# Kernel optimization log

Measured on AMD Instinct MI355X. Metric: run time of the kernel, lower is better.

## Reference

```python
import jax, jax.numpy as jnp
import numpy as np

DIM = 128      # embedding dim (c)
HEAD_DIM = 32
NH = DIM // HEAD_DIM          # 4 mLSTM heads
INNER = 256                    # round_up(2*DIM, 64)
DH = INNER // NH               # 64 per-head dim
K = 4                          # causal conv kernel size
BS = 4                         # qkv_proj_blocksize
NB = INNER // BS               # 64 block-diagonal qkv blocks
B, T, H, W = 8, 16, 32, 32


def setup_inputs() -> dict:
    key = jax.random.key(0)
    ks = jax.random.split(key, 12)
    s = 0.02
    return {
        "x": jax.random.normal(ks[0], (B, DIM, T, H, W), jnp.float32),
        "W_up": jax.random.normal(ks[1], (DIM, 2 * INNER), jnp.float32) * s,
        "conv_w": jax.random.normal(ks[2], (K, 1, INNER), jnp.float32) * s,  # depthwise causal conv (WIO)
        "conv_b": jnp.zeros((INNER,), jnp.float32),
        "Wq": jax.random.normal(ks[3], (NB, BS, BS), jnp.float32) * s,  # block-diag headwise linear
        "Wk": jax.random.normal(ks[4], (NB, BS, BS), jnp.float32) * s,
        "Wv": jax.random.normal(ks[5], (NB, BS, BS), jnp.float32) * s,
        "ig_w": jax.random.normal(ks[6], (3 * INNER, NH), jnp.float32) * s,
        "ig_b": jnp.zeros((NH,), jnp.float32),
        "fg_w": jax.random.normal(ks[7], (3 * INNER, NH), jnp.float32) * s,
        "fg_b": jnp.zeros((NH,), jnp.float32),
        "ln_w": jnp.ones((INNER,), jnp.float32),   # multi-head layernorm scale
        "skip": jnp.ones((INNER,), jnp.float32),   # learnable skip
        "W_down": jax.random.normal(ks[8], (INNER, DIM), jnp.float32) * s,
    }


def _headwise(y, Wh):
    # block-diagonal linear: y [B,S,INNER] split into NB blocks of BS
    Bx, S, _ = y.shape
    yb = y.reshape(Bx, S, NB, BS)
    return jnp.einsum('bsni,noi->bsno', yb, Wh).reshape(Bx, S, INNER)


def _mlstm_parallel(q, k, v, ig, fg):
    # q,k,v: [B,NH,S,DH]; ig,fg (gate preacts): [B,NH,S]
    S = q.shape[2]
    log_f = jax.nn.log_sigmoid(fg)
    lf_cum = jnp.concatenate(
        [jnp.zeros_like(log_f[..., :1]), jnp.cumsum(log_f, axis=-1)], axis=-1)  # [B,NH,S+1]
    logfg = lf_cum[..., 1:, None] - lf_cum[..., None, 1:]                      # [B,NH,S,S]
    mask = jnp.tril(jnp.ones((S, S), bool))
    logfg = jnp.where(mask, logfg, -jnp.inf)
    log_D = logfg + ig[..., None, :]
    max_log_D = jnp.max(log_D, axis=-1, keepdims=True)
    Dmat = jnp.exp(log_D - max_log_D)
    qk = jnp.einsum('bhsd,bhtd->bhst', q, k) / jnp.sqrt(jnp.float32(q.shape[-1]))
    C = qk * Dmat
    normalizer = jnp.maximum(jnp.abs(C.sum(-1, keepdims=True)), jnp.exp(-max_log_D))
    return jnp.einsum('bhst,bhtd->bhsd', C / (normalizer + 1e-6), v)


def _forward(x, W_up, conv_w, conv_b, Wq, Wk, Wv, ig_w, ig_b, fg_w, fg_b, ln_w, skip, W_down):
    b, c, t, hh, ww = x.shape
    xs = jnp.transpose(x, (0, 3, 4, 2, 1)).reshape(b * hh * ww, t, c)  # (b h w) t c
    up = xs @ W_up
    x_m, z = jnp.split(up, 2, axis=-1)                                  # [Bx,S,INNER] each
    # depthwise causal conv + swish
    xc = jax.lax.conv_general_dilated(
        x_m, conv_w, (1,), [(K - 1, 0)],
        dimension_numbers=('NWC', 'WIO', 'NWC'), feature_group_count=INNER) + conv_b
    xc = jax.nn.silu(xc)
    q = _headwise(xc, Wq)
    k = _headwise(xc, Wk)
    v = _headwise(x_m, Wv)
    if_in = jnp.concatenate([q, k, v], axis=-1)
    ig = if_in @ ig_w + ig_b                                            # [Bx,S,NH]
    fg = if_in @ fg_w + fg_b
    Bx, S = q.shape[0], q.shape[1]
    qh = q.reshape(Bx, S, NH, DH).transpose(0, 2, 1, 3)
    kh = k.reshape(Bx, S, NH, DH).transpose(0, 2, 1, 3)
    vh = v.reshape(Bx, S, NH, DH).transpose(0, 2, 1, 3)
    ht = _mlstm_parallel(qh, kh, vh, ig.transpose(0, 2, 1), fg.transpose(0, 2, 1))  # [Bx,NH,S,DH]
    # multi-head (group) layernorm over DH, weight only
    mu = ht.mean(-1, keepdims=True)
    var = ht.var(-1, keepdims=True)
    hn = (ht - mu) / jnp.sqrt(var + 1e-5) * ln_w.reshape(NH, DH)[None, :, None, :]
    hn = hn.transpose(0, 2, 1, 3).reshape(Bx, S, INNER)
    h_state = (hn + skip * xc) * jax.nn.silu(z)
    out = h_state @ W_down                                              # [Bx,S,DIM]
    return out.reshape(b, hh, ww, t, c).transpose(0, 4, 3, 1, 2)        # b c t h w


def reference(x, W_up, conv_w, conv_b, Wq, Wk, Wv, ig_w, ig_b, fg_w, fg_b, ln_w, skip, W_down):
    return _forward(x, W_up, conv_w, conv_b, Wq, Wk, Wv, ig_w, ig_b, fg_w, fg_b, ln_w, skip, W_down)
```

## Files before the change

kernel.cpp:

```cpp
#include <hip/hip_runtime.h>
#include <hip/hip_bf16.h>
#include <cmath>


typedef __attribute__((ext_vector_type(8))) short short8;
typedef __attribute__((ext_vector_type(4))) short short4v;
typedef __attribute__((ext_vector_type(4))) float f32x4;
typedef unsigned short ushort_t;

static __device__ __forceinline__ float siluf(float v) {
  return v / (1.0f + __expf(-v));
}
static __device__ __forceinline__ float logsigf(float v) {
  return fminf(v, 0.f) - log1pf(__expf(-fabsf(v)));
}
static __device__ __forceinline__ float sel4(float4 w, int idx) {
  float r = w.x;
  r = (idx == 1) ? w.y : r;
  r = (idx == 2) ? w.z : r;
  r = (idx == 3) ? w.w : r;
  return r;
}
static __device__ __forceinline__ ushort_t f2bf(float x) {
  unsigned u = __float_as_uint(x);
  return (ushort_t)((u + 0x7fffu + ((u >> 16) & 1u)) >> 16);
}
static __device__ __forceinline__ float bf2f(ushort_t h) {
  return __uint_as_float(((unsigned)h) << 16);
}
static __device__ __forceinline__ ushort2 pk2bf(float a, float b) {
  union { __hip_bfloat162 v; ushort2 u; } cv;
  cv.v = __float22bfloat162_rn(make_float2(a, b));
  return cv.u;
}

__global__ __launch_bounds__(256)
void prep_w(const float* __restrict__ Wup, const float* __restrict__ Wd,
            const float* __restrict__ igw, const float* __restrict__ fgw,
            ushort_t* __restrict__ wt_hi, ushort_t* __restrict__ wt_lo,
            ushort_t* __restrict__ wdt_hi, ushort_t* __restrict__ wdt_lo,
            ushort_t* __restrict__ wgf)
{
  const int g = blockIdx.x * 256 + threadIdx.x;
  if (g < 65536) {
    const int c = g >> 9, j = g & 511;
    const float w = Wup[g];
    const ushort_t h = f2bf(w);
    wt_hi[j*128 + c] = h;
    wt_lo[j*128 + c] = f2bf(w - bf2f(h));
  } else if (g < 98304) {
    const int g2 = g - 65536;
    const int j = g2 >> 7, c = g2 & 127;
    const float w = Wd[g2];
    const ushort_t h = f2bf(w);
    wdt_hi[c*256 + j] = h;
    wdt_lo[c*256 + j] = f2bf(w - bf2f(h));
  } else if (g < 110592) {
    const int e = g - 98304;
    const int kc = e >> 9;
    const int lane = (e >> 3) & 63;
    const int i = e & 7;
    const int n = lane & 15;
    const int kq = kc*32 + (lane >> 4)*8 + i;
    float val = 0.f;
    if (n < 4)      val = igw[kq*4 + n];
    else if (n < 8) val = fgw[kq*4 + (n - 4)];
    wgf[e] = f2bf(val);
  }
}

#define AS 72

__global__ __launch_bounds__(256, 3)
void up_gemm(const float* __restrict__ x,
             const ushort_t* __restrict__ wt_hi, const ushort_t* __restrict__ wt_lo,
             ushort_t* __restrict__ xmb, ushort_t* __restrict__ szb)
{
  __shared__ ushort_t sAhi[128*AS];
  __shared__ ushort_t sAlo[128*AS];

  const int tid = threadIdx.x;
  const int hw0 = blockIdx.x * 128;
  const int j0  = blockIdx.y * 128;
  const int bt  = blockIdx.z;
  const int b   = bt >> 4, t = bt & 15;

  const int wv = tid >> 6;
  const int wm = wv >> 1, wn = wv & 1;
  const int ln = tid & 63;
  const int lm = ln & 15;
  const int q  = ln >> 4;

  const int hwL = tid & 127;
  const int cg  = tid >> 7;

  f32x4 acc[4][4];
  #pragma unroll
  for (int i = 0; i < 4; ++i)
    #pragma unroll
    for (int k = 0; k < 4; ++k) acc[i][k] = (f32x4){0.f, 0.f, 0.f, 0.f};

  for (int stage = 0; stage < 2; ++stage) {
    float xv[8][4];
    {
      const float* xb = &x[((b*128 + stage*64)*16 + t)*1024 + hw0 + hwL];
      #pragma unroll
      for (int p = 0; p < 8; ++p) {
        const float* xp = xb + (p*8 + cg*4)*16384;
        xv[p][0] = xp[0];
        xv[p][1] = xp[16384];
        xv[p][2] = xp[32768];
        xv[p][3] = xp[49152];
      }
    }
    #pragma unroll
    for (int p = 0; p < 8; ++p) {
      const int cl = p*8 + cg*4;
      const float v0 = xv[p][0], v1 = xv[p][1], v2 = xv[p][2], v3 = xv[p][3];
      const ushort2 h01 = pk2bf(v0, v1);
      const ushort2 h23 = pk2bf(v2, v3);
      const ushort2 l01 = pk2bf(v0 - bf2f(h01.x), v1 - bf2f(h01.y));
      const ushort2 l23 = pk2bf(v2 - bf2f(h23.x), v3 - bf2f(h23.y));
      *(ushort4*)&sAhi[hwL*AS + cl] = make_ushort4(h01.x, h01.y, h23.x, h23.y);
      *(ushort4*)&sAlo[hwL*AS + cl] = make_ushort4(l01.x, l01.y, l23.x, l23.y);
    }
    __syncthreads();

    #pragma unroll
    for (int s = 0; s < 2; ++s) {
      const int kc = s*32 + q*8;
      const int kg = stage*64 + kc;
      short8 bh[4], bl[4];
      #pragma unroll
      for (int nt = 0; nt < 4; ++nt) {
        const int jr = j0 + wn*64 + nt*16 + lm;
        bh[nt] = *(const short8*)&wt_hi[jr*128 + kg];
        bl[nt] = *(const short8*)&wt_lo[jr*128 + kg];
      }
      #pragma unroll
      for (int mt = 0; mt < 4; ++mt) {
        const int ao = (wm*64 + mt*16 + lm)*AS + kc;
        const short8 ah = *(const short8*)&sAhi[ao];
        const short8 al = *(const short8*)&sAlo[ao];
        #pragma unroll
        for (int nt = 0; nt < 4; ++nt) {
          acc[mt][nt] = __builtin_amdgcn_mfma_f32_16x16x32_bf16(ah, bh[nt], acc[mt][nt], 0, 0, 0);
          acc[mt][nt] = __builtin_amdgcn_mfma_f32_16x16x32_bf16(ah, bl[nt], acc[mt][nt], 0, 0, 0);
          acc[mt][nt] = __builtin_amdgcn_mfma_f32_16x16x32_bf16(al, bh[nt], acc[mt][nt], 0, 0, 0);
        }
      }
    }
    __syncthreads();
  }

  const bool isz = (j0 >= 256);
  #pragma unroll
  for (int mt = 0; mt < 4; ++mt) {
    #pragma unroll
    for (int nt = 0; nt < 4; ++nt) {
      const int jc = j0 + wn*64 + nt*16 + lm;
      #pragma unroll
      for (int r = 0; r < 4; ++r) {
        const int rowg = bt*1024 + hw0 + wm*64 + mt*16 + q*4 + r;
        const float v = acc[mt][nt][r];
        if (!isz) xmb[rowg*256 + jc] = f2bf(v);
        else      szb[rowg*256 + (jc - 256)] = f2bf(siluf(v));
      }
    }
  }
}

#define SQ 264
#define SXC 260

__global__ __launch_bounds__(256, 4)
void seq_kernel(const ushort_t* __restrict__ xm_ws,
                ushort_t* szh,
                const float* __restrict__ conv_w, const float* __restrict__ conv_b,
                const float* __restrict__ Wq, const float* __restrict__ Wk,
                const float* __restrict__ Wv,
                const ushort_t* __restrict__ wgf,
                const float* __restrict__ igb, const float* __restrict__ fgb,
                const float* __restrict__ lnw, const float* __restrict__ skipw)
{
  __shared__ __align__(16) ushort_t q_lds[16*SQ];
  __shared__ __align__(16) ushort_t k_lds[16*SQ];
  __shared__ __align__(16) ushort_t v_lds[16*SQ];
  __shared__ __align__(16) ushort_t xc_lds[16*SXC];
  __shared__ __align__(16) ushort_t p_lds[4*16*36];
  __shared__ __align__(16) float s_gpart[512];
  __shared__ float s_ig[64];
  __shared__ float s_lf[64];

  const int tid = threadIdx.x;
  const int j   = tid;
  const int l2  = j & 3;
  const int seq = blockIdx.x;
  const int rbase = (seq >> 10) * 16384 + (seq & 1023);

  const int w    = tid >> 6;
  const int ln   = tid & 63;
  const int g    = ln >> 4;
  const int lc   = ln & 15;
  const int hb2  = w * 64;

  const float4 wq4 = *(const float4*)&Wq[j*4];
  const float4 wk4 = *(const float4*)&Wk[j*4];
  const float4 wv4 = *(const float4*)&Wv[j*4];
  float wqp[4], wkp[4], wvp[4];
  #pragma unroll
  for (int d = 0; d < 4; ++d) {
    const int idx = l2 ^ d;
    wqp[d] = sel4(wq4, idx);
    wkp[d] = sel4(wk4, idx);
    wvp[d] = sel4(wv4, idx);
  }
  const float cw0 = conv_w[j],     cw1 = conv_w[256+j];
  const float cw2 = conv_w[512+j], cw3 = conv_w[768+j];
  const float cb  = conv_b[j];

  float p1 = 0.f, p2 = 0.f, p3 = 0.f;
  #pragma unroll
  for (int t = 0; t < 16; ++t) {
    const float m = bf2f(xm_ws[(rbase + t*1024)*256 + j]);
    const float pre = cw0*p3 + cw1*p2 + cw2*p1 + cw3*m + cb;
    const float x = siluf(pre);
    p3 = p2; p2 = p1; p1 = m;
    const float x1 = __shfl_xor(x, 1), x2 = __shfl_xor(x, 2), x3 = __shfl_xor(x, 3);
    const float m1 = __shfl_xor(m, 1), m2 = __shfl_xor(m, 2), m3 = __shfl_xor(m, 3);
    const float qv = x*wqp[0] + x1*wqp[1] + x2*wqp[2] + x3*wqp[3];
    const float kv = x*wkp[0] + x1*wkp[1] + x2*wkp[2] + x3*wkp[3];
    const float vv = m*wvp[0] + m1*wvp[1] + m2*wvp[2] + m3*wvp[3];
    q_lds [t*SQ  + j] = f2bf(qv);
    k_lds [t*SQ  + j] = f2bf(kv);
    v_lds [t*SQ  + j] = f2bf(vv);
    xc_lds[t*SXC + j] = f2bf(x);
  }
  __syncthreads();

  f32x4 gacc = (f32x4){0.f, 0.f, 0.f, 0.f};
  #pragma unroll
  for (int c6 = 0; c6 < 6; ++c6) {
    const int kc = w*6 + c6;
    const ushort_t* yb = (kc < 8) ? q_lds : (kc < 16) ? k_lds : v_lds;
    const int klocal = (kc & 7)*32;
    const short8 ya = *(const short8*)&yb[lc*SQ + klocal + g*8];
    const short8 wb = *(const short8*)&wgf[(kc*64 + ln)*8];
    gacc = __builtin_amdgcn_mfma_f32_16x16x32_bf16(ya, wb, gacc, 0, 0, 0);
  }
  f32x4 qkacc = (f32x4){0.f, 0.f, 0.f, 0.f};
  {
    const short8 qa0 = *(const short8*)&q_lds[lc*SQ + hb2 + g*8];
    const short8 qa1 = *(const short8*)&q_lds[lc*SQ + hb2 + 32 + g*8];
    const short8 kb0 = *(const short8*)&k_lds[lc*SQ + hb2 + g*8];
    const short8 kb1 = *(const short8*)&k_lds[lc*SQ + hb2 + 32 + g*8];
    qkacc = __builtin_amdgcn_mfma_f32_16x16x32_bf16(qa0, kb0, qkacc, 0, 0, 0);
    qkacc = __builtin_amdgcn_mfma_f32_16x16x32_bf16(qa1, kb1, qkacc, 0, 0, 0);
  }
  if (lc < 8) {
    #pragma unroll
    for (int r = 0; r < 4; ++r)
      s_gpart[w*128 + (g*4 + r)*8 + lc] = gacc[r];
  }
  __syncthreads();

  if (tid < 128) {
    const int t = tid >> 3, n = tid & 7;
    const float s = s_gpart[t*8+n] + s_gpart[128 + t*8+n]
                  + s_gpart[256 + t*8+n] + s_gpart[384 + t*8+n];
    if (n < 4) s_ig[t*4 + n] = s + igb[n];
    else       s_lf[t*4 + (n-4)] = logsigf(s + fgb[n-4]);
  }
  __syncthreads();

  float* s_lfc = s_gpart;
  if (tid < 4) {
    float run = 0.f;
    s_lfc[tid] = 0.f;
    #pragma unroll
    for (int t = 0; t < 16; ++t) { run += s_lf[t*4 + tid]; s_lfc[(t+1)*4 + tid] = run; }
  }
  __syncthreads();

  {
    const int tcol = lc;
    const float lfc_t1 = s_lfc[(tcol+1)*4 + w];
    const float igt    = s_ig[tcol*4 + w];
    float ld[4], mloc[4];
    #pragma unroll
    for (int r = 0; r < 4; ++r) {
      const int s = g*4 + r;
      const float lfs = s_lfc[(s+1)*4 + w];
      ld[r] = (tcol <= s) ? (lfs - lfc_t1 + igt) : -INFINITY;
      mloc[r] = ld[r];
    }
    #pragma unroll
    for (int off = 1; off < 16; off <<= 1) {
      #pragma unroll
      for (int r = 0; r < 4; ++r) mloc[r] = fmaxf(mloc[r], __shfl_xor(mloc[r], off));
    }
    float cs[4], rsum[4];
    #pragma unroll
    for (int r = 0; r < 4; ++r) {
      const int s = g*4 + r;
      cs[r] = (tcol <= s) ? (qkacc[r] * 0.125f) * __expf(ld[r] - mloc[r]) : 0.f;
      rsum[r] = cs[r];
    }
    #pragma unroll
    for (int off = 1; off < 16; off <<= 1) {
      #pragma unroll
      for (int r = 0; r < 4; ++r) rsum[r] += __shfl_xor(rsum[r], off);
    }
    #pragma unroll
    for (int r = 0; r < 4; ++r) {
      const float denom = fmaxf(fabsf(rsum[r]), __expf(-mloc[r])) + 1e-6f;
      const float pv = cs[r] / denom;
      p_lds[(w*16 + g*4 + r)*36 + tcol] = f2bf(pv);
    }
  }
  __syncthreads();

  f32x4 oacc[4];
  #pragma unroll
  for (int c = 0; c < 4; ++c) oacc[c] = (f32x4){0.f, 0.f, 0.f, 0.f};
  {
    const int tb = g*8;
    short8 pa = (short8){0,0,0,0,0,0,0,0};
    if (tb < 16) {
      const short4v plo = *(const short4v*)&p_lds[(w*16 + lc)*36 + tb];
      const short4v phi = *(const short4v*)&p_lds[(w*16 + lc)*36 + tb + 4];
      pa[0]=plo[0]; pa[1]=plo[1]; pa[2]=plo[2]; pa[3]=plo[3];
      pa[4]=phi[0]; pa[5]=phi[1]; pa[6]=phi[2]; pa[7]=phi[3];
    }
    #pragma unroll
    for (int c = 0; c < 4; ++c) {
      short8 vb;
      #pragma unroll
      for (int i = 0; i < 8; ++i)
        vb[i] = (short)v_lds[((tb + i) & 15)*SQ + hb2 + c*16 + lc];
      oacc[c] = __builtin_amdgcn_mfma_f32_16x16x32_bf16(pa, vb, oacc[c], 0, 0, 0);
    }
  }

  float lnc[4], skc[4];
  #pragma unroll
  for (int c = 0; c < 4; ++c) {
    const int ch = hb2 + c*16 + lc;
    lnc[c] = lnw[ch];
    skc[c] = skipw[ch];
  }
  #pragma unroll
  for (int r = 0; r < 4; ++r) {
    const int s = g*4 + r;
    float tot = oacc[0][r] + oacc[1][r] + oacc[2][r] + oacc[3][r];
    #pragma unroll
    for (int off = 1; off < 16; off <<= 1) tot += __shfl_xor(tot, off);
    const float mu = tot * (1.f/64.f);
    float var = 0.f;
    #pragma unroll
    for (int c = 0; c < 4; ++c) { const float d = oacc[c][r] - mu; var += d*d; }
    #pragma unroll
    for (int off = 1; off < 16; off <<= 1) var += __shfl_xor(var, off);
    const float rstd = rsqrtf(var * (1.f/64.f) + 1e-5f);
    #pragma unroll
    for (int c = 0; c < 4; ++c) {
      const int ch = hb2 + c*16 + lc;
      const float hn = (oacc[c][r] - mu) * rstd * lnc[c];
      const float xcv = bf2f(xc_lds[s*SXC + ch]);
      q_lds[s*SQ + ch] = f2bf(hn + skc[c]*xcv);
    }
  }
  __syncthreads();

  #pragma unroll
  for (int s = 0; s < 16; ++s) {
    const long long og = (long long)(rbase + s*1024)*256 + tid;
    const float szv = bf2f(szh[og]);
    const float hv  = bf2f(q_lds[s*SQ + tid]);
    szh[og] = f2bf(hv * szv);
  }
}

__global__ __launch_bounds__(256, 3)
void down_gemm(const ushort_t* __restrict__ hb,
               const ushort_t* __restrict__ wdt_hi, const ushort_t* __restrict__ wdt_lo,
               float* __restrict__ out)
{
  const int tid = threadIdx.x;
  const int hw0 = blockIdx.x * 128;
  const int bt  = blockIdx.z;
  const int bq  = bt >> 4, tq = bt & 15;
  const int rowbase = bt*1024 + hw0;

  const int wv = tid >> 6;
  const int wm = wv >> 1, wn = wv & 1;
  const int ln = tid & 63;
  const int lm = ln & 15;
  const int q  = ln >> 4;

  f32x4 acc[4][4];
  #pragma unroll
  for (int i = 0; i < 4; ++i)
    #pragma unroll
    for (int k = 0; k < 4; ++k) acc[i][k] = (f32x4){0.f, 0.f, 0.f, 0.f};

  #pragma unroll 2
  for (int kc = 0; kc < 256; kc += 32) {
    const int kq = kc + q*8;
    short8 ah[4], al[4];
    #pragma unroll
    for (int mt = 0; mt < 4; ++mt) {
      const int c = wm*64 + mt*16 + lm;
      ah[mt] = *(const short8*)&wdt_hi[c*256 + kq];
      al[mt] = *(const short8*)&wdt_lo[c*256 + kq];
    }
    #pragma unroll
    for (int nt = 0; nt < 4; ++nt) {
      const int n = wn*64 + nt*16 + lm;
      const short8 bf = *(const short8*)&hb[(rowbase + n)*256 + kq];
      #pragma unroll
      for (int mt = 0; mt < 4; ++mt) {
        acc[mt][nt] = __builtin_amdgcn_mfma_f32_16x16x32_bf16(ah[mt], bf, acc[mt][nt], 0, 0, 0);
        acc[mt][nt] = __builtin_amdgcn_mfma_f32_16x16x32_bf16(al[mt], bf, acc[mt][nt], 0, 0, 0);
      }
    }
  }

  #pragma unroll
  for (int mt = 0; mt < 4; ++mt) {
    #pragma unroll
    for (int nt = 0; nt < 4; ++nt) {
      const int hw = hw0 + wn*64 + nt*16 + lm;
      #pragma unroll
      for (int r = 0; r < 4; ++r) {
        const int c = wm*64 + mt*16 + q*4 + r;
        out[((bq*128 + c)*16 + tq)*1024 + hw] = acc[mt][nt][r];
      }
    }
  }
}

extern "C" void kernel_launch(void* const* d_in, const int* in_sizes, int n_in,
                              void* d_out, int out_size, void* d_ws, size_t ws_size,
                              hipStream_t stream)
{
  const float* x      = (const float*)d_in[0];
  const float* Wup    = (const float*)d_in[1];
  const float* conv_w = (const float*)d_in[2];
  const float* conv_b = (const float*)d_in[3];
  const float* Wq     = (const float*)d_in[4];
  const float* Wk     = (const float*)d_in[5];
  const float* Wv     = (const float*)d_in[6];
  const float* igw    = (const float*)d_in[7];
  const float* igb    = (const float*)d_in[8];
  const float* fgw    = (const float*)d_in[9];
  const float* fgb    = (const float*)d_in[10];
  const float* lnw    = (const float*)d_in[11];
  const float* skipw  = (const float*)d_in[12];
  const float* Wd     = (const float*)d_in[13];
  float* out = (float*)d_out;

  ushort_t* xmb    = (ushort_t*)d_ws;
  ushort_t* szb    = xmb + 33554432;
  ushort_t* wt_hi  = (ushort_t*)((char*)d_ws + 134217728);
  ushort_t* wt_lo  = wt_hi + 65536;
  ushort_t* wdt_hi = wt_lo + 65536;
  ushort_t* wdt_lo = wdt_hi + 32768;
  ushort_t* wgf    = wdt_lo + 32768;

  prep_w<<<432, 256, 0, stream>>>(Wup, Wd, igw, fgw,
                                  wt_hi, wt_lo, wdt_hi, wdt_lo, wgf);
  up_gemm<<<dim3(8, 4, 128), 256, 0, stream>>>(x, wt_hi, wt_lo, xmb, szb);
  seq_kernel<<<8192, 256, 0, stream>>>(xmb, szb,
                                       conv_w, conv_b, Wq, Wk, Wv,
                                       wgf, igb, fgb, lnw, skipw);
  down_gemm<<<dim3(8, 1, 128), 256, 0, stream>>>(szb, wdt_hi, wdt_lo, out);
}
```

Measured before the change: 388.5 us.

## Fuse down-projection GEMM into seq_kernel and remap block-to-sequence order

The separate down_gemm kernel is removed. Each seq_kernel block now multiplies its 16x256 gated hidden state, held in LDS, by the down-projection weights using MFMA and writes the fp32 output directly. This drops the bf16 h_state write and re-read through global memory and one kernel launch. Block IDs are also remapped so adjacent blocks cover different batch slices. In exchange, the output stores are strided (one hw element per row across 1024-float strides), so writes are uncoalesced, and every block re-reads the down weights.

Result: slower. 439.3 us (+13.1%).

```diff
diff --git a/kernel.cpp b/kernel.cpp
--- a/kernel.cpp
+++ b/kernel.cpp
@@ -175,11 +175,13 @@
 
 __global__ __launch_bounds__(256, 4)
 void seq_kernel(const ushort_t* __restrict__ xm_ws,
-                ushort_t* szh,
+                const ushort_t* __restrict__ szb,
+                float* __restrict__ out,
                 const float* __restrict__ conv_w, const float* __restrict__ conv_b,
                 const float* __restrict__ Wq, const float* __restrict__ Wk,
                 const float* __restrict__ Wv,
                 const ushort_t* __restrict__ wgf,
+                const ushort_t* __restrict__ wdt_hi, const ushort_t* __restrict__ wdt_lo,
                 const float* __restrict__ igb, const float* __restrict__ fgb,
                 const float* __restrict__ lnw, const float* __restrict__ skipw)
 {
@@ -195,8 +197,11 @@
   const int tid = threadIdx.x;
   const int j   = tid;
   const int l2  = j & 3;
-  const int seq = blockIdx.x;
-  const int rbase = (seq >> 10) * 16384 + (seq & 1023);
+  const int bid = blockIdx.x;
+  const int seq = (bid & 7) * 1024 + (bid >> 3);
+  const int bq  = seq >> 10;
+  const int hw  = seq & 1023;
+  const int rbase = bq * 16384 + hw;
 
   const int w    = tid >> 6;
   const int ln   = tid & 63;
@@ -375,66 +380,35 @@
   #pragma unroll
   for (int s = 0; s < 16; ++s) {
     const long long og = (long long)(rbase + s*1024)*256 + tid;
-    const float szv = bf2f(szh[og]);
+    const float szv = bf2f(szb[og]);
     const float hv  = bf2f(q_lds[s*SQ + tid]);
-    szh[og] = f2bf(hv * szv);
-  }
-}
-
-__global__ __launch_bounds__(256, 3)
-void down_gemm(const ushort_t* __restrict__ hb,
-               const ushort_t* __restrict__ wdt_hi, const ushort_t* __restrict__ wdt_lo,
-               float* __restrict__ out)
-{
-  const int tid = threadIdx.x;
-  const int hw0 = blockIdx.x * 128;
-  const int bt  = blockIdx.z;
-  const int bq  = bt >> 4, tq = bt & 15;
-  const int rowbase = bt*1024 + hw0;
-
-  const int wv = tid >> 6;
-  const int wm = wv >> 1, wn = wv & 1;
-  const int ln = tid & 63;
-  const int lm = ln & 15;
-  const int q  = ln >> 4;
-
-  f32x4 acc[4][4];
-  #pragma unroll
-  for (int i = 0; i < 4; ++i)
-    #pragma unroll
-    for (int k = 0; k < 4; ++k) acc[i][k] = (f32x4){0.f, 0.f, 0.f, 0.f};
-
-  #pragma unroll 2
-  for (int kc = 0; kc < 256; kc += 32) {
-    const int kq = kc + q*8;
-    short8 ah[4], al[4];
-    #pragma unroll
-    for (int mt = 0; mt < 4; ++mt) {
-      const int c = wm*64 + mt*16 + lm;
-      ah[mt] = *(const short8*)&wdt_hi[c*256 + kq];
-      al[mt] = *(const short8*)&wdt_lo[c*256 + kq];
-    }
-    #pragma unroll
-    for (int nt = 0; nt < 4; ++nt) {
-      const int n = wn*64 + nt*16 + lm;
-      const short8 bf = *(const short8*)&hb[(rowbase + n)*256 + kq];
-      #pragma unroll
-      for (int mt = 0; mt < 4; ++mt) {
-        acc[mt][nt] = __builtin_amdgcn_mfma_f32_16x16x32_bf16(ah[mt], bf, acc[mt][nt], 0, 0, 0);
-        acc[mt][nt] = __builtin_amdgcn_mfma_f32_16x16x32_bf16(al[mt], bf, acc[mt][nt], 0, 0, 0);
-      }
-    }
-  }
-
-  #pragma unroll
-  for (int mt = 0; mt < 4; ++mt) {
-    #pragma unroll
-    for (int nt = 0; nt < 4; ++nt) {
-      const int hw = hw0 + wn*64 + nt*16 + lm;
+    q_lds[s*SQ + tid] = f2bf(hv * szv);
+  }
+  __syncthreads();
+
+  {
+    f32x4 accd[2];
+    accd[0] = (f32x4){0.f, 0.f, 0.f, 0.f};
+    accd[1] = (f32x4){0.f, 0.f, 0.f, 0.f};
+    const int c00 = w*32;
+    #pragma unroll 2
+    for (int kc = 0; kc < 256; kc += 32) {
+      const short8 bfr = *(const short8*)&q_lds[lc*SQ + kc + g*8];
+      #pragma unroll
+      for (int mt = 0; mt < 2; ++mt) {
+        const int c = c00 + mt*16 + lc;
+        const short8 ah = *(const short8*)&wdt_hi[c*256 + kc + g*8];
+        const short8 al = *(const short8*)&wdt_lo[c*256 + kc + g*8];
+        accd[mt] = __builtin_amdgcn_mfma_f32_16x16x32_bf16(ah, bfr, accd[mt], 0, 0, 0);
+        accd[mt] = __builtin_amdgcn_mfma_f32_16x16x32_bf16(al, bfr, accd[mt], 0, 0, 0);
+      }
+    }
+    #pragma unroll
+    for (int mt = 0; mt < 2; ++mt) {
       #pragma unroll
       for (int r = 0; r < 4; ++r) {
-        const int c = wm*64 + mt*16 + q*4 + r;
-        out[((bq*128 + c)*16 + tq)*1024 + hw] = acc[mt][nt][r];
+        const int c = c00 + mt*16 + g*4 + r;
+        out[((long long)(bq*128 + c)*16 + lc)*1024 + hw] = accd[mt][r];
       }
     }
   }
@@ -471,8 +445,8 @@
   prep_w<<<432, 256, 0, stream>>>(Wup, Wd, igw, fgw,
                                   wt_hi, wt_lo, wdt_hi, wdt_lo, wgf);
   up_gemm<<<dim3(8, 4, 128), 256, 0, stream>>>(x, wt_hi, wt_lo, xmb, szb);
-  seq_kernel<<<8192, 256, 0, stream>>>(xmb, szb,
+  seq_kernel<<<8192, 256, 0, stream>>>(xmb, szb, out,
                                        conv_w, conv_b, Wq, Wk, Wv,
-                                       wgf, igb, fgb, lnw, skipw);
-  down_gemm<<<dim3(8, 1, 128), 256, 0, stream>>>(szb, wdt_hi, wdt_lo, out);
-}
+                                       wgf, wdt_hi, wdt_lo,
+                                       igb, fgb, lnw, skipw);
+}
```
